# Kernel tuning notes

Hardware: AMD Instinct MI355X
Metric: run time of the kernel (lower is better)

The kernel has to match this reference:

```python
import jax, jax.numpy as jnp
import numpy as np

N, E, F, C, L = 100000, 1000000, 128, 64, 4
NS_CONV = 0.2   # GATv2 internal leaky_relu negative_slope
NS_ACT = 0.01   # nn.LeakyReLU() default activation slope
EPS = 1e-5      # BatchNorm1d / GraphNorm eps


def _lrelu(x, s):
    return jnp.where(x >= 0, x, s * x)


def setup_inputs() -> dict:
    key = jax.random.key(0)
    ks = jax.random.split(key, 8)
    sc = lambda k, shape: jax.random.normal(k, shape, jnp.float32) * 0.1
    return {
        "x": jax.random.normal(ks[0], (N, F), jnp.float32),
        "src": jax.random.randint(ks[1], (E,), 0, N, jnp.int32),
        "dst": jax.random.randint(ks[2], (E,), 0, N, jnp.int32),
        "bn_w": jnp.ones((F,), jnp.float32),
        "bn_b": jnp.zeros((F,), jnp.float32),
        "bn_mean": jnp.zeros((F,), jnp.float32),
        "bn_var": jnp.ones((F,), jnp.float32),
        "in_W": sc(ks[3], (C, F)),
        "in_b": jnp.zeros((C,), jnp.float32),
        "lin_W": sc(ks[4], (L, C, C)),
        "lin_b": jnp.zeros((L, C), jnp.float32),
        "att": sc(ks[5], (L, C)),
        "conv_b": jnp.zeros((L, C), jnp.float32),
        "gn_w": jnp.ones((L, C), jnp.float32),
        "gn_b": jnp.zeros((L, C), jnp.float32),
        "gn_ms": jnp.ones((L, C), jnp.float32),
    }


def reference(x, src, dst, bn_w, bn_b, bn_mean, bn_var, in_W, in_b,
              lin_W, lin_b, att, conv_b, gn_w, gn_b, gn_ms):
    n = x.shape[0]
    # GATv2Conv(add_self_loops=True): append one self-loop per node
    loops = jnp.arange(n, dtype=src.dtype)
    s_idx = jnp.concatenate([src, loops])  # [E'] = E + N
    d_idx = jnp.concatenate([dst, loops])

    # eval-mode BatchNorm1d with running stats, then input Linear + LeakyReLU
    h = (x - bn_mean) / jnp.sqrt(bn_var + EPS) * bn_w + bn_b
    h = _lrelu(h @ in_W.T + in_b, NS_ACT)  # [N, C]

    alphas = []
    for l in range(L):
        # GATv2Conv, heads=1, share_weights=True (x_l = x_r = lin(x))
        z = h @ lin_W[l].T + lin_b[l]                 # [N, C]
        e = _lrelu(z[s_idx] + z[d_idx], NS_CONV)      # [E', C]
        score = e @ att[l]                            # [E']
        # segment softmax over destination nodes (every segment has a self-loop)
        m = jax.ops.segment_max(score, d_idx, num_segments=n)
        ex = jnp.exp(score - m[d_idx])
        denom = jax.ops.segment_sum(ex, d_idx, num_segments=n)
        a = ex / (denom[d_idx] + 1e-16)               # [E'] attention weights
        alphas.append(a)
        # aggregate messages alpha * z_src, add conv bias
        h = jax.ops.segment_sum(a[:, None] * z[s_idx], d_idx, num_segments=n) + conv_b[l]
        # GraphNorm (batch=None -> single graph: global mean/var)
        mu = h.mean(0)
        o = h - gn_ms[l] * mu
        var = (o * o).mean(0)
        h = gn_w[l] * o / jnp.sqrt(var + EPS) + gn_b[l]
        # activation; dropout(p=0.3) is identity in eval mode
        h = _lrelu(h, NS_ACT)
    # default path (acummulate=False, return_one=False): (x, x, stacked attn)
    return h, h, jnp.stack(alphas, 0)  # ([N,C], [N,C], [L, E+N])
```

## Files before the change

kernel.cpp:

```cpp
#include <hip/hip_runtime.h>
#include <math.h>
#include <stdint.h>

#define NN 100000
#define NE 1000000
#define EP 1100000
#define FI 128
#define CC 64
#define NLAY 4
#define NXCD 8
#define NSLICE (NN / NXCD)
#define NS_CONV 0.2f
#define NS_ACT  0.01f
#define EPSV 1e-5f

__device__ __forceinline__ float lrelu(float x, float s) { return x >= 0.f ? x : s * x; }
__device__ __forceinline__ int srcOf(const int* s, int e) { return e < NE ? s[e] : e - NE; }
__device__ __forceinline__ int dstOf(const int* d, int e) { return e < NE ? d[e] : e - NE; }

__global__ __launch_bounds__(256) void k_count(const int* __restrict__ dst, int* __restrict__ counts) {
    int slice = blockIdx.x & (NXCD - 1);
    int blk   = blockIdx.x >> 3;
    int nblk  = gridDim.x >> 3;
    int lo = slice * NSLICE, hi = lo + NSLICE;
    for (int e = blk * 256 + threadIdx.x; e < EP; e += nblk * 256) {
        int d = dstOf(dst, e);
        if (d >= lo && d < hi) atomicAdd(&counts[d], 1);
    }
}

__global__ void k_scan1(const int* __restrict__ counts, int* __restrict__ bsum) {
    int t = threadIdx.x;
    int base = blockIdx.x * 1024 + t * 4;
    int s = 0;
#pragma unroll
    for (int k = 0; k < 4; k++) { int i = base + k; if (i < NN) s += counts[i]; }
#pragma unroll
    for (int off = 32; off; off >>= 1) s += __shfl_down(s, off);
    __shared__ int ws[4];
    if ((t & 63) == 0) ws[t >> 6] = s;
    __syncthreads();
    if (t == 0) bsum[blockIdx.x] = ws[0] + ws[1] + ws[2] + ws[3];
}

__global__ void k_scan2(const int* __restrict__ bsum, int* __restrict__ bbase,
                        int* __restrict__ offs, int nb) {
    int t = threadIdx.x;
    int v = (t < nb) ? bsum[t] : 0;
    int x = v;
#pragma unroll
    for (int off = 1; off < 64; off <<= 1) { int y = __shfl_up(x, off); if ((t & 63) >= off) x += y; }
    __shared__ int wtot[2];
    if ((t & 63) == 63) wtot[t >> 6] = x;
    __syncthreads();
    if (t >= 64) x += wtot[0];
    if (t < nb) bbase[t] = x - v;
    if (t == 127) offs[NN] = x;
}

__global__ void k_scan3(const int* __restrict__ counts, const int* __restrict__ bbase,
                        int* __restrict__ offs, int* __restrict__ cursor) {
    int t = threadIdx.x;
    int base = blockIdx.x * 1024 + t * 4;
    int v[4]; int tsum = 0;
#pragma unroll
    for (int k = 0; k < 4; k++) { int i = base + k; v[k] = (i < NN) ? counts[i] : 0; tsum += v[k]; }
    int x = tsum;
#pragma unroll
    for (int off = 1; off < 64; off <<= 1) { int y = __shfl_up(x, off); if ((t & 63) >= off) x += y; }
    __shared__ int ws[4];
    if ((t & 63) == 63) ws[t >> 6] = x;
    __syncthreads();
    int w = t >> 6; int wb = 0;
    for (int i = 0; i < w; i++) wb += ws[i];
    int run = (x - tsum) + wb + bbase[blockIdx.x];
#pragma unroll
    for (int k = 0; k < 4; k++) {
        int i = base + k;
        if (i < NN) { offs[i] = run; cursor[i] = run; run += v[k]; }
    }
}

__global__ __launch_bounds__(256) void k_fill(const int* __restrict__ src, const int* __restrict__ dst,
                                              int* __restrict__ cursor, int2* __restrict__ elist2) {
    int slice = blockIdx.x & (NXCD - 1);
    int blk   = blockIdx.x >> 3;
    int nblk  = gridDim.x >> 3;
    int lo = slice * NSLICE, hi = lo + NSLICE;
    for (int e = blk * 256 + threadIdx.x; e < EP; e += nblk * 256) {
        int d = dstOf(dst, e);
        if (d >= lo && d < hi) {
            int p = atomicAdd(&cursor[d], 1);
            elist2[p] = make_int2(e, srcOf(src, e));
        }
    }
}

__global__ void k_fold(const float* __restrict__ bn_w, const float* __restrict__ bn_b,
                       const float* __restrict__ bn_mean, const float* __restrict__ bn_var,
                       const float* __restrict__ in_W, const float* __restrict__ in_b,
                       float* __restrict__ W2t, float* __restrict__ b2) {
    int t = blockIdx.x * 256 + threadIdx.x;
    if (t < FI * CC) {
        int f = t >> 6, c = t & 63;
        float scale = bn_w[f] * rsqrtf(bn_var[f] + EPSV);
        W2t[f * CC + c] = in_W[c * FI + f] * scale;
    }
    if (t < CC) {
        float acc = in_b[t];
        for (int f = 0; f < FI; f++) {
            float scale = bn_w[f] * rsqrtf(bn_var[f] + EPSV);
            acc += in_W[t * FI + f] * (bn_b[f] - bn_mean[f] * scale);
        }
        b2[t] = acc;
    }
}

__global__ __launch_bounds__(128) void k_in(const float* __restrict__ x, const float* __restrict__ W2t,
                                            const float* __restrict__ b2, float* __restrict__ h) {
    __shared__ float sW[FI * CC];
    __shared__ float sx[64 * (FI + 1)];
    for (int i = threadIdx.x; i < FI * CC; i += 128) sW[i] = W2t[i];
    int lane = threadIdx.x & 63;
    int wv = threadIdx.x >> 6;
    int cg = lane & 15;
    int ng = lane >> 4;
    float4 bias = ((const float4*)b2)[cg];
    int nchunks = (NN + 63) / 64;
    for (int chunk = blockIdx.x; chunk < nchunks; chunk += gridDim.x) {
        int n0 = chunk * 64;
        __syncthreads();
        for (int i = threadIdx.x; i < 64 * (FI / 4); i += 128) {
            int r = i >> 5, f4 = i & 31;
            int nn = n0 + r;
            float4 v = (nn < NN) ? ((const float4*)x)[(size_t)nn * (FI / 4) + f4]
                                 : make_float4(0.f, 0.f, 0.f, 0.f);
            float* dp = &sx[r * (FI + 1) + f4 * 4];
            dp[0] = v.x; dp[1] = v.y; dp[2] = v.z; dp[3] = v.w;
        }
        __syncthreads();
        int nbase = wv * 32 + ng * 8;
        float a[8][4];
#pragma unroll
        for (int k = 0; k < 8; k++) { a[k][0] = bias.x; a[k][1] = bias.y; a[k][2] = bias.z; a[k][3] = bias.w; }
        const float* hb = &sx[nbase * (FI + 1)];
#pragma unroll 4
        for (int f = 0; f < FI; f++) {
            float4 w = *(const float4*)&sW[f * CC + (cg << 2)];
#pragma unroll
            for (int k = 0; k < 8; k++) {
                float hv = hb[k * (FI + 1) + f];
                a[k][0] = fmaf(hv, w.x, a[k][0]);
                a[k][1] = fmaf(hv, w.y, a[k][1]);
                a[k][2] = fmaf(hv, w.z, a[k][2]);
                a[k][3] = fmaf(hv, w.w, a[k][3]);
            }
        }
#pragma unroll
        for (int k = 0; k < 8; k++) {
            int n = n0 + nbase + k;
            if (n < NN) {
                float4 o = make_float4(lrelu(a[k][0], NS_ACT), lrelu(a[k][1], NS_ACT),
                                       lrelu(a[k][2], NS_ACT), lrelu(a[k][3], NS_ACT));
                ((float4*)h)[(size_t)n * 16 + cg] = o;
            }
        }
    }
}

__global__ __launch_bounds__(256) void k_z(const float* __restrict__ h, const float* __restrict__ Wl,
                                           const float* __restrict__ bl, const float* __restrict__ AB,
                                           int do_norm, float* __restrict__ z) {
    __shared__ float sW[CC * CC];
    __shared__ float sh[128 * (CC + 1)];
    __shared__ float sA[CC], sB[CC];
    if (threadIdx.x < CC) {
        sA[threadIdx.x] = do_norm ? AB[threadIdx.x] : 1.f;
        sB[threadIdx.x] = do_norm ? AB[CC + threadIdx.x] : 0.f;
    }
    for (int i = threadIdx.x; i < CC * CC; i += 256) {
        int f = i >> 6, c = i & 63;
        sW[f * CC + c] = Wl[c * CC + f];
    }
    int lane = threadIdx.x & 63;
    int wv = threadIdx.x >> 6;
    int cg = lane & 15;
    int ng = lane >> 4;
    float4 bias = ((const float4*)bl)[cg];
    int nchunks = (NN + 127) / 128;
    for (int chunk = blockIdx.x; chunk < nchunks; chunk += gridDim.x) {
        int n0 = chunk * 128;
        __syncthreads();
        for (int i = threadIdx.x; i < 128 * (CC / 4); i += 256) {
            int r = i >> 4, f4 = i & 15;
            int nn = n0 + r;
            float4 v = (nn < NN) ? ((const float4*)h)[(size_t)nn * 16 + f4]
                                 : make_float4(0.f, 0.f, 0.f, 0.f);
            float* dp = &sh[r * (CC + 1) + f4 * 4];
            if (do_norm) {
                int c0 = f4 * 4;
                dp[0] = lrelu(sA[c0 + 0] * v.x + sB[c0 + 0], NS_ACT);
                dp[1] = lrelu(sA[c0 + 1] * v.y + sB[c0 + 1], NS_ACT);
                dp[2] = lrelu(sA[c0 + 2] * v.z + sB[c0 + 2], NS_ACT);
                dp[3] = lrelu(sA[c0 + 3] * v.w + sB[c0 + 3], NS_ACT);
            } else {
                dp[0] = v.x; dp[1] = v.y; dp[2] = v.z; dp[3] = v.w;
            }
        }
        __syncthreads();
        int nbase = wv * 32 + ng * 8;
        float a[8][4];
#pragma unroll
        for (int k = 0; k < 8; k++) { a[k][0] = bias.x; a[k][1] = bias.y; a[k][2] = bias.z; a[k][3] = bias.w; }
        const float* hb = &sh[nbase * (CC + 1)];
#pragma unroll 4
        for (int f = 0; f < CC; f++) {
            float4 w = *(const float4*)&sW[f * CC + (cg << 2)];
#pragma unroll
            for (int k = 0; k < 8; k++) {
                float hv = hb[k * (CC + 1) + f];
                a[k][0] = fmaf(hv, w.x, a[k][0]);
                a[k][1] = fmaf(hv, w.y, a[k][1]);
                a[k][2] = fmaf(hv, w.z, a[k][2]);
                a[k][3] = fmaf(hv, w.w, a[k][3]);
            }
        }
#pragma unroll
        for (int k = 0; k < 8; k++) {
            int n = n0 + nbase + k;
            if (n < NN) {
                float4 o = make_float4(a[k][0], a[k][1], a[k][2], a[k][3]);
                ((float4*)z)[(size_t)n * 16 + cg] = o;
            }
        }
    }
}

__global__ __launch_bounds__(256) void k_agg(const float* __restrict__ z, const float* __restrict__ att_l,
                                             const int2* __restrict__ elist2, const int* __restrict__ offs,
                                             const float* __restrict__ convb,
                                             float* __restrict__ h, float* __restrict__ ex_csr,
                                             float* __restrict__ alpha) {
    int w = threadIdx.x >> 6, lane = threadIdx.x & 63;
    int n = blockIdx.x * 4 + w;
    if (n >= NN) return;
    int g = lane >> 4;
    int q = lane & 15;
    int base = offs[n], end = offs[n + 1];
    const float4* z4 = (const float4*)z;
    float4 attq = ((const float4*)att_l)[q];
    float4 zd = z4[(size_t)n * 16 + q];
    float den = 0.f;
    float4 acc = make_float4(0.f, 0.f, 0.f, 0.f);

    int j = base + g;
    float4 zs = make_float4(0.f, 0.f, 0.f, 0.f);
    if (j < end) { int2 es = elist2[j]; zs = z4[(size_t)es.y * 16 + q]; }
    while (j < end) {
        float4 zc = zs;
        int jn = j + 4;
        if (jn < end) { int2 es = elist2[jn]; zs = z4[(size_t)es.y * 16 + q]; }
        float p = lrelu(zc.x + zd.x, NS_CONV) * attq.x
                + lrelu(zc.y + zd.y, NS_CONV) * attq.y
                + lrelu(zc.z + zd.z, NS_CONV) * attq.z
                + lrelu(zc.w + zd.w, NS_CONV) * attq.w;
        p += __shfl_xor(p, 1);
        p += __shfl_xor(p, 2);
        p += __shfl_xor(p, 4);
        p += __shfl_xor(p, 8);
        float ex = __expf(p);
        if (q == 0) ex_csr[j] = ex;
        den += ex;
        acc.x = fmaf(ex, zc.x, acc.x);
        acc.y = fmaf(ex, zc.y, acc.y);
        acc.z = fmaf(ex, zc.z, acc.z);
        acc.w = fmaf(ex, zc.w, acc.w);
        j = jn;
    }
#pragma unroll
    for (int msk = 16; msk <= 32; msk <<= 1) {
        den   += __shfl_xor(den, msk);
        acc.x += __shfl_xor(acc.x, msk);
        acc.y += __shfl_xor(acc.y, msk);
        acc.z += __shfl_xor(acc.z, msk);
        acc.w += __shfl_xor(acc.w, msk);
    }
    float inv = 1.f / (den + 1e-16f);
    if (g == 0) {
        float4 cb = ((const float4*)convb)[q];
        float4 o = make_float4(fmaf(acc.x, inv, cb.x), fmaf(acc.y, inv, cb.y),
                               fmaf(acc.z, inv, cb.z), fmaf(acc.w, inv, cb.w));
        ((float4*)h)[(size_t)n * 16 + q] = o;
    }
    for (int jj = base + lane; jj < end; jj += 64) {
        int eid = elist2[jj].x;
        alpha[eid] = ex_csr[jj] * inv;
    }
}

__global__ __launch_bounds__(256) void k_r12(const float* __restrict__ h,
                                             double* __restrict__ pS, double* __restrict__ pQ,
                                             const float* __restrict__ gn_w_l, const float* __restrict__ gn_b_l,
                                             const float* __restrict__ gn_ms_l, float* __restrict__ AB,
                                             int* __restrict__ done) {
    int c = threadIdx.x & 63, w = threadIdx.x >> 6;
    double s = 0.0, q = 0.0;
    for (int n = blockIdx.x * 4 + w; n < NN; n += gridDim.x * 4) {
        float v = h[(size_t)n * CC + c];
        s += (double)v; q += (double)v * (double)v;
    }
    __shared__ double ls[4][64], lq[4][64];
    ls[w][c] = s; lq[w][c] = q;
    __syncthreads();
    if (w == 0) {
        pS[blockIdx.x * CC + c] = ls[0][c] + ls[1][c] + ls[2][c] + ls[3][c];
        pQ[blockIdx.x * CC + c] = lq[0][c] + lq[1][c] + lq[2][c] + lq[3][c];
    }
    __threadfence();
    __shared__ int amLast;
    if (threadIdx.x == 0) amLast = (atomicAdd(done, 1) == gridDim.x - 1) ? 1 : 0;
    __syncthreads();
    if (!amLast) return;
    __threadfence();
    double fs = 0.0, fq = 0.0;
    for (int b = w; b < gridDim.x; b += 4) {
        fs += pS[b * CC + c];
        fq += pQ[b * CC + c];
    }
    ls[w][c] = fs; lq[w][c] = fq;
    __syncthreads();
    if (threadIdx.x < CC) {
        double S = ls[0][c] + ls[1][c] + ls[2][c] + ls[3][c];
        double Q = lq[0][c] + lq[1][c] + lq[2][c] + lq[3][c];
        double mu = S / (double)NN;
        double ms = (double)gn_ms_l[c];
        double var = Q / (double)NN - 2.0 * ms * mu * mu + ms * ms * mu * mu;
        float A = gn_w_l[c] * rsqrtf((float)var + EPSV);
        float B = gn_b_l[c] - A * (float)(ms * mu);
        AB[c] = A; AB[CC + c] = B;
    }
}

__global__ void k_out(const float* __restrict__ h, const float* __restrict__ AB,
                      float* __restrict__ o0, float* __restrict__ o1) {
    int i = blockIdx.x * 256 + threadIdx.x;
    if (i >= NN * 16) return;
    int cg = i & 15;
    float4 hv = ((const float4*)h)[i];
    float4 A = ((const float4*)AB)[cg];
    float4 B = ((const float4*)(AB + CC))[cg];
    float4 o = make_float4(lrelu(A.x * hv.x + B.x, NS_ACT), lrelu(A.y * hv.y + B.y, NS_ACT),
                           lrelu(A.z * hv.z + B.z, NS_ACT), lrelu(A.w * hv.w + B.w, NS_ACT));
    ((float4*)o0)[i] = o;
    ((float4*)o1)[i] = o;
}

extern "C" void kernel_launch(void* const* d_in, const int* in_sizes, int n_in,
                              void* d_out, int out_size, void* d_ws, size_t ws_size,
                              hipStream_t stream) {
    const float* x       = (const float*)d_in[0];
    const int*   src     = (const int*)d_in[1];
    const int*   dst     = (const int*)d_in[2];
    const float* bn_w    = (const float*)d_in[3];
    const float* bn_b    = (const float*)d_in[4];
    const float* bn_mean = (const float*)d_in[5];
    const float* bn_var  = (const float*)d_in[6];
    const float* in_W    = (const float*)d_in[7];
    const float* in_b    = (const float*)d_in[8];
    const float* lin_W   = (const float*)d_in[9];
    const float* lin_b   = (const float*)d_in[10];
    const float* att     = (const float*)d_in[11];
    const float* conv_b  = (const float*)d_in[12];
    const float* gn_w    = (const float*)d_in[13];
    const float* gn_b    = (const float*)d_in[14];
    const float* gn_ms   = (const float*)d_in[15];

    float* out = (float*)d_out;
    float* out_h0 = out;
    float* out_h1 = out + (size_t)NN * CC;
    float* out_alpha = out + (size_t)2 * NN * CC;

    const int NB_R = 256;

    char* wsp = (char*)d_ws;
    double* pS    = (double*)wsp;
    double* pQ    = pS + NB_R * CC;
    float* h      = (float*)(pQ + NB_R * CC);
    float* z      = h + (size_t)NN * CC;
    float* exbuf  = z + (size_t)NN * CC;
    int2* elist2  = (int2*)(exbuf + EP);
    int* counts   = (int*)(elist2 + EP);
    int* done     = counts + NN;
    int* offs     = done + 8;
    int* cursor   = offs + (NN + 4);
    int* bsum     = cursor + NN;
    int* bbase    = bsum + 128;
    float* W2t    = (float*)(bbase + 128);
    float* b2     = W2t + FI * CC;
    float* AB     = b2 + CC;

    const int NB_SCAN = (NN + 1023) / 1024;

    hipMemsetAsync(counts, 0, (NN + 8) * sizeof(int), stream);
    k_count<<<1024, 256, 0, stream>>>(dst, counts);
    k_scan1<<<NB_SCAN, 256, 0, stream>>>(counts, bsum);
    k_scan2<<<1, 128, 0, stream>>>(bsum, bbase, offs, NB_SCAN);
    k_scan3<<<NB_SCAN, 256, 0, stream>>>(counts, bbase, offs, cursor);
    k_fill<<<1024, 256, 0, stream>>>(src, dst, cursor, elist2);

    k_fold<<<(FI * CC + 255) / 256, 256, 0, stream>>>(bn_w, bn_b, bn_mean, bn_var, in_W, in_b, W2t, b2);
    k_in<<<(NN + 63) / 64, 128, 0, stream>>>(x, W2t, b2, h);

    for (int l = 0; l < NLAY; l++) {
        const float* Wl      = lin_W + (size_t)l * CC * CC;
        const float* bl      = lin_b + (size_t)l * CC;
        const float* att_l   = att + (size_t)l * CC;
        const float* convb_l = conv_b + (size_t)l * CC;
        const float* gn_w_l  = gn_w + (size_t)l * CC;
        const float* gn_b_l  = gn_b + (size_t)l * CC;
        const float* gn_ms_l = gn_ms + (size_t)l * CC;
        float* alpha_l = out_alpha + (size_t)l * EP;

        k_z<<<(NN + 127) / 128, 256, 0, stream>>>(h, Wl, bl, AB, l > 0 ? 1 : 0, z);
        k_agg<<<(NN + 3) / 4, 256, 0, stream>>>(z, att_l, elist2, offs, convb_l, h, exbuf, alpha_l);
        k_r12<<<NB_R, 256, 0, stream>>>(h, pS, pQ, gn_w_l, gn_b_l, gn_ms_l, AB, done + l);
    }

    k_out<<<(NN * 16 + 255) / 256, 256, 0, stream>>>(h, AB, out_h0, out_h1);
}
```

Measured before the change: 942.8 us.

## Store z in bf16, add online softmax, remap agg blocks per XCD, fold BN into k_in

The z buffer now holds bf16 instead of fp32, which halves the bytes moved by the random-gather traffic in k_agg. The aggregation switches to an online max-stabilised softmax: it stores raw scores and recomputes exp when writing alpha. It also remaps block indices so each XCD works on a contiguous node slice, matching the CSR fill. The separate k_fold kernel is removed and BatchNorm is applied inside k_in. Together these cut gather bandwidth and one launch, at the cost of bf16 precision loss in z and extra exp work.

```diff
diff --git a/kernel.cpp b/kernel.cpp
--- a/kernel.cpp
+++ b/kernel.cpp
@@ -1,4 +1,5 @@
 #include <hip/hip_runtime.h>
+#include <hip/hip_bf16.h>
 #include <math.h>
 #include <stdint.h>
 
@@ -13,10 +14,19 @@
 #define NS_CONV 0.2f
 #define NS_ACT  0.01f
 #define EPSV 1e-5f
+#define NEG_INF (-3.402823466e38f)
 
 __device__ __forceinline__ float lrelu(float x, float s) { return x >= 0.f ? x : s * x; }
 __device__ __forceinline__ int srcOf(const int* s, int e) { return e < NE ? s[e] : e - NE; }
 __device__ __forceinline__ int dstOf(const int* d, int e) { return e < NE ? d[e] : e - NE; }
+
+__device__ __forceinline__ float b2f(unsigned short u) {
+    union { unsigned int i; float f; } v; v.i = ((unsigned int)u) << 16; return v.f;
+}
+__device__ __forceinline__ unsigned short f2b(float f) {
+    __hip_bfloat16 b = __float2bfloat16(f);
+    return *reinterpret_cast<unsigned short*>(&b);
+}
 
 __global__ __launch_bounds__(256) void k_count(const int* __restrict__ dst, int* __restrict__ counts) {
     int slice = blockIdx.x & (NXCD - 1);
@@ -96,36 +106,29 @@
     }
 }
 
-__global__ void k_fold(const float* __restrict__ bn_w, const float* __restrict__ bn_b,
-                       const float* __restrict__ bn_mean, const float* __restrict__ bn_var,
-                       const float* __restrict__ in_W, const float* __restrict__ in_b,
-                       float* __restrict__ W2t, float* __restrict__ b2) {
-    int t = blockIdx.x * 256 + threadIdx.x;
-    if (t < FI * CC) {
-        int f = t >> 6, c = t & 63;
-        float scale = bn_w[f] * rsqrtf(bn_var[f] + EPSV);
-        W2t[f * CC + c] = in_W[c * FI + f] * scale;
-    }
-    if (t < CC) {
-        float acc = in_b[t];
-        for (int f = 0; f < FI; f++) {
-            float scale = bn_w[f] * rsqrtf(bn_var[f] + EPSV);
-            acc += in_W[t * FI + f] * (bn_b[f] - bn_mean[f] * scale);
-        }
-        b2[t] = acc;
-    }
-}
-
-__global__ __launch_bounds__(128) void k_in(const float* __restrict__ x, const float* __restrict__ W2t,
-                                            const float* __restrict__ b2, float* __restrict__ h) {
+__global__ __launch_bounds__(128) void k_in(const float* __restrict__ x,
+                                            const float* __restrict__ bn_w, const float* __restrict__ bn_b,
+                                            const float* __restrict__ bn_mean, const float* __restrict__ bn_var,
+                                            const float* __restrict__ in_W, const float* __restrict__ in_b,
+                                            float* __restrict__ h) {
     __shared__ float sW[FI * CC];
     __shared__ float sx[64 * (FI + 1)];
-    for (int i = threadIdx.x; i < FI * CC; i += 128) sW[i] = W2t[i];
+    __shared__ float sScale[FI], sShift[FI];
+    if (threadIdx.x < FI) {
+        int f = threadIdx.x;
+        float sc = bn_w[f] * rsqrtf(bn_var[f] + EPSV);
+        sScale[f] = sc;
+        sShift[f] = bn_b[f] - bn_mean[f] * sc;
+    }
+    for (int i = threadIdx.x; i < FI * CC; i += 128) {
+        int f = i >> 6, c = i & 63;
+        sW[f * CC + c] = in_W[c * FI + f];
+    }
     int lane = threadIdx.x & 63;
     int wv = threadIdx.x >> 6;
     int cg = lane & 15;
     int ng = lane >> 4;
-    float4 bias = ((const float4*)b2)[cg];
+    float4 bias = ((const float4*)in_b)[cg];
     int nchunks = (NN + 63) / 64;
     for (int chunk = blockIdx.x; chunk < nchunks; chunk += gridDim.x) {
         int n0 = chunk * 64;
@@ -135,8 +138,12 @@
             int nn = n0 + r;
             float4 v = (nn < NN) ? ((const float4*)x)[(size_t)nn * (FI / 4) + f4]
                                  : make_float4(0.f, 0.f, 0.f, 0.f);
-            float* dp = &sx[r * (FI + 1) + f4 * 4];
-            dp[0] = v.x; dp[1] = v.y; dp[2] = v.z; dp[3] = v.w;
+            int c0 = f4 * 4;
+            float* dp = &sx[r * (FI + 1) + c0];
+            dp[0] = v.x * sScale[c0 + 0] + sShift[c0 + 0];
+            dp[1] = v.y * sScale[c0 + 1] + sShift[c0 + 1];
+            dp[2] = v.z * sScale[c0 + 2] + sShift[c0 + 2];
+            dp[3] = v.w * sScale[c0 + 3] + sShift[c0 + 3];
         }
         __syncthreads();
         int nbase = wv * 32 + ng * 8;
@@ -170,7 +177,7 @@
 
 __global__ __launch_bounds__(256) void k_z(const float* __restrict__ h, const float* __restrict__ Wl,
                                            const float* __restrict__ bl, const float* __restrict__ AB,
-                                           int do_norm, float* __restrict__ z) {
+                                           int do_norm, ushort4* __restrict__ z16) {
     __shared__ float sW[CC * CC];
     __shared__ float sh[128 * (CC + 1)];
     __shared__ float sA[CC], sB[CC];
@@ -229,37 +236,39 @@
         for (int k = 0; k < 8; k++) {
             int n = n0 + nbase + k;
             if (n < NN) {
-                float4 o = make_float4(a[k][0], a[k][1], a[k][2], a[k][3]);
-                ((float4*)z)[(size_t)n * 16 + cg] = o;
+                ushort4 o;
+                o.x = f2b(a[k][0]); o.y = f2b(a[k][1]); o.z = f2b(a[k][2]); o.w = f2b(a[k][3]);
+                z16[(size_t)n * 16 + cg] = o;
             }
         }
     }
 }
 
-__global__ __launch_bounds__(256) void k_agg(const float* __restrict__ z, const float* __restrict__ att_l,
+__global__ __launch_bounds__(256) void k_agg(const ushort4* __restrict__ z16, const float* __restrict__ att_l,
                                              const int2* __restrict__ elist2, const int* __restrict__ offs,
                                              const float* __restrict__ convb,
-                                             float* __restrict__ h, float* __restrict__ ex_csr,
+                                             float* __restrict__ h, float* __restrict__ score_csr,
                                              float* __restrict__ alpha) {
+    int wg = (blockIdx.x & 7) * (25000 / 8) + (blockIdx.x >> 3);
     int w = threadIdx.x >> 6, lane = threadIdx.x & 63;
-    int n = blockIdx.x * 4 + w;
+    int n = wg * 4 + w;
     if (n >= NN) return;
     int g = lane >> 4;
     int q = lane & 15;
     int base = offs[n], end = offs[n + 1];
-    const float4* z4 = (const float4*)z;
     float4 attq = ((const float4*)att_l)[q];
-    float4 zd = z4[(size_t)n * 16 + q];
-    float den = 0.f;
+    ushort4 zdu = z16[(size_t)n * 16 + q];
+    float4 zd = make_float4(b2f(zdu.x), b2f(zdu.y), b2f(zdu.z), b2f(zdu.w));
+    float m = NEG_INF, den = 0.f;
     float4 acc = make_float4(0.f, 0.f, 0.f, 0.f);
 
     int j = base + g;
-    float4 zs = make_float4(0.f, 0.f, 0.f, 0.f);
-    if (j < end) { int2 es = elist2[j]; zs = z4[(size_t)es.y * 16 + q]; }
+    ushort4 zsu = make_ushort4(0, 0, 0, 0);
+    if (j < end) { int2 es = elist2[j]; zsu = z16[(size_t)es.y * 16 + q]; }
     while (j < end) {
-        float4 zc = zs;
+        float4 zc = make_float4(b2f(zsu.x), b2f(zsu.y), b2f(zsu.z), b2f(zsu.w));
         int jn = j + 4;
-        if (jn < end) { int2 es = elist2[jn]; zs = z4[(size_t)es.y * 16 + q]; }
+        if (jn < end) { int2 es = elist2[jn]; zsu = z16[(size_t)es.y * 16 + q]; }
         float p = lrelu(zc.x + zd.x, NS_CONV) * attq.x
                 + lrelu(zc.y + zd.y, NS_CONV) * attq.y
                 + lrelu(zc.z + zd.z, NS_CONV) * attq.z
@@ -268,22 +277,35 @@
         p += __shfl_xor(p, 2);
         p += __shfl_xor(p, 4);
         p += __shfl_xor(p, 8);
-        float ex = __expf(p);
-        if (q == 0) ex_csr[j] = ex;
-        den += ex;
-        acc.x = fmaf(ex, zc.x, acc.x);
-        acc.y = fmaf(ex, zc.y, acc.y);
-        acc.z = fmaf(ex, zc.z, acc.z);
-        acc.w = fmaf(ex, zc.w, acc.w);
+        if (q == 0) score_csr[j] = p;
+        float mn = fmaxf(m, p);
+        float s0 = __expf(m - mn);
+        float ex = __expf(p - mn);
+        den = den * s0 + ex;
+        acc.x = acc.x * s0 + ex * zc.x;
+        acc.y = acc.y * s0 + ex * zc.y;
+        acc.z = acc.z * s0 + ex * zc.z;
+        acc.w = acc.w * s0 + ex * zc.w;
+        m = mn;
         j = jn;
     }
 #pragma unroll
     for (int msk = 16; msk <= 32; msk <<= 1) {
-        den   += __shfl_xor(den, msk);
-        acc.x += __shfl_xor(acc.x, msk);
-        acc.y += __shfl_xor(acc.y, msk);
-        acc.z += __shfl_xor(acc.z, msk);
-        acc.w += __shfl_xor(acc.w, msk);
+        float mo  = __shfl_xor(m, msk);
+        float dno = __shfl_xor(den, msk);
+        float aox = __shfl_xor(acc.x, msk);
+        float aoy = __shfl_xor(acc.y, msk);
+        float aoz = __shfl_xor(acc.z, msk);
+        float aow = __shfl_xor(acc.w, msk);
+        float mn = fmaxf(m, mo);
+        float s1 = __expf(m - mn);
+        float s2 = __expf(mo - mn);
+        den = den * s1 + dno * s2;
+        acc.x = acc.x * s1 + aox * s2;
+        acc.y = acc.y * s1 + aoy * s2;
+        acc.z = acc.z * s1 + aoz * s2;
+        acc.w = acc.w * s1 + aow * s2;
+        m = mn;
     }
     float inv = 1.f / (den + 1e-16f);
     if (g == 0) {
@@ -294,7 +316,7 @@
     }
     for (int jj = base + lane; jj < end; jj += 64) {
         int eid = elist2[jj].x;
-        alpha[eid] = ex_csr[jj] * inv;
+        alpha[eid] = __expf(score_csr[jj] - m) * inv;
     }
 }
 
@@ -385,19 +407,17 @@
     char* wsp = (char*)d_ws;
     double* pS    = (double*)wsp;
     double* pQ    = pS + NB_R * CC;
-    float* h      = (float*)(pQ + NB_R * CC);
-    float* z      = h + (size_t)NN * CC;
-    float* exbuf  = z + (size_t)NN * CC;
-    int2* elist2  = (int2*)(exbuf + EP);
-    int* counts   = (int*)(elist2 + EP);
+    int2* elist2  = (int2*)(pQ + NB_R * CC);
+    float* h      = (float*)(elist2 + EP);
+    float* score  = h + (size_t)NN * CC;
+    ushort4* z16  = (ushort4*)(score + EP);
+    int* counts   = (int*)(z16 + (size_t)NN * 16);
     int* done     = counts + NN;
     int* offs     = done + 8;
     int* cursor   = offs + (NN + 4);
     int* bsum     = cursor + NN;
     int* bbase    = bsum + 128;
-    float* W2t    = (float*)(bbase + 128);
-    float* b2     = W2t + FI * CC;
-    float* AB     = b2 + CC;
+    float* AB     = (float*)(bbase + 128);
 
     const int NB_SCAN = (NN + 1023) / 1024;
 
@@ -408,8 +428,7 @@
     k_scan3<<<NB_SCAN, 256, 0, stream>>>(counts, bbase, offs, cursor);
     k_fill<<<1024, 256, 0, stream>>>(src, dst, cursor, elist2);
 
-    k_fold<<<(FI * CC + 255) / 256, 256, 0, stream>>>(bn_w, bn_b, bn_mean, bn_var, in_W, in_b, W2t, b2);
-    k_in<<<(NN + 63) / 64, 128, 0, stream>>>(x, W2t, b2, h);
+    k_in<<<(NN + 63) / 64, 128, 0, stream>>>(x, bn_w, bn_b, bn_mean, bn_var, in_W, in_b, h);
 
     for (int l = 0; l < NLAY; l++) {
         const float* Wl      = lin_W + (size_t)l * CC * CC;
@@ -421,8 +440,8 @@
         const float* gn_ms_l = gn_ms + (size_t)l * CC;
         float* alpha_l = out_alpha + (size_t)l * EP;
 
-        k_z<<<(NN + 127) / 128, 256, 0, stream>>>(h, Wl, bl, AB, l > 0 ? 1 : 0, z);
-        k_agg<<<(NN + 3) / 4, 256, 0, stream>>>(z, att_l, elist2, offs, convb_l, h, exbuf, alpha_l);
+        k_z<<<(NN + 127) / 128, 256, 0, stream>>>(h, Wl, bl, AB, l > 0 ? 1 : 0, z16);
+        k_agg<<<(NN + 3) / 4, 256, 0, stream>>>(z16, att_l, elist2, offs, convb_l, h, score, alpha_l);
         k_r12<<<NB_R, 256, 0, stream>>>(h, pS, pQ, gn_w_l, gn_b_l, gn_ms_l, AB, done + l);
     }
 
```

After: 951.6 us. No clear change (+0.9%).
